# Kernel optimization log

Hardware: AMD Instinct MI355X
Metric: run time of the kernel (lower is better)

Reference implementation:

```python
import jax, jax.numpy as jnp
import numpy as np

D_MODEL = 256
N_HEADS = 8
N_LEVELS = 4
NUM_POINTS_LIST = [4, 4, 4, 4]
SUM_POINTS = sum(NUM_POINTS_LIST)
TOTAL_POINTS = N_HEADS * SUM_POINTS
HEAD_DIM = D_MODEL // N_HEADS
OFFSET_SCALE = 0.5
SPATIAL_SHAPES = np.array([[80, 80], [40, 40], [20, 20], [10, 10]], dtype=np.int64)


def setup_inputs() -> dict:
    key = jax.random.key(0)
    ks = jax.random.split(key, 7)
    B, NQ = 16, 300
    seq = int((SPATIAL_SHAPES[:, 0] * SPATIAL_SHAPES[:, 1]).sum())  # 8500
    s = 1.0 / np.sqrt(D_MODEL)
    return {
        'hidden_states': jax.random.normal(ks[0], (B, NQ, D_MODEL), jnp.float32),
        'encoder_hidden_states': jax.random.normal(ks[1], (B, seq, D_MODEL), jnp.float32),
        'reference_points': jax.random.uniform(ks[2], (B, NQ, 1, 4), jnp.float32, 0.05, 0.95),
        'spatial_shapes': SPATIAL_SHAPES,
        'w_off': jax.random.uniform(ks[3], (TOTAL_POINTS * 2, D_MODEL), jnp.float32, -s, s),
        'b_off': jax.random.uniform(ks[4], (TOTAL_POINTS * 2,), jnp.float32, -s, s),
        'w_attn': jax.random.uniform(ks[5], (TOTAL_POINTS, D_MODEL), jnp.float32, -s, s),
        'b_attn': jax.random.uniform(ks[6], (TOTAL_POINTS,), jnp.float32, -s, s),
    }


def _grid_sample_zeros(img_flat, H, W, gx, gy):
    # img_flat: [N, H*W, C]; gx, gy: [N, Q, P] unnormalized pixel coords.
    # Bilinear, padding_mode='zeros', align_corners=False semantics of torch.grid_sample.
    x0 = jnp.floor(gx)
    y0 = jnp.floor(gy)
    wx = (gx - x0)[..., None]
    wy = (gy - y0)[..., None]
    x0i = x0.astype(jnp.int32)
    y0i = y0.astype(jnp.int32)

    def gather(xi, yi):
        valid = (xi >= 0) & (xi < W) & (yi >= 0) & (yi < H)
        idx = jnp.clip(yi, 0, H - 1) * W + jnp.clip(xi, 0, W - 1)
        N = img_flat.shape[0]
        v = jnp.take_along_axis(img_flat, idx.reshape(N, -1)[..., None], axis=1)
        v = v.reshape(idx.shape + (img_flat.shape[-1],))
        return v * valid[..., None]

    v00 = gather(x0i, y0i)
    v01 = gather(x0i + 1, y0i)
    v10 = gather(x0i, y0i + 1)
    v11 = gather(x0i + 1, y0i + 1)
    top = v00 * (1 - wx) + v01 * wx
    bot = v10 * (1 - wx) + v11 * wx
    return top * (1 - wy) + bot * wy  # [N, Q, P, C]


def reference(hidden_states, encoder_hidden_states, reference_points, spatial_shapes, w_off, b_off, w_attn, b_attn):
    B, NQ, _ = hidden_states.shape
    seq = encoder_hidden_states.shape[1]
    shapes = np.asarray(spatial_shapes)

    value = encoder_hidden_states.reshape(B, seq, N_HEADS, HEAD_DIM)

    off = (hidden_states @ w_off.T + b_off).reshape(B, NQ, N_HEADS, SUM_POINTS, 2)
    attn = jax.nn.softmax((hidden_states @ w_attn.T + b_attn).reshape(B, NQ, N_HEADS, SUM_POINTS), axis=-1)

    # reference_points: [B, NQ, 1, 4] (cx, cy, w, h) in [0,1]
    nps = jnp.asarray(np.repeat([1.0 / n for n in NUM_POINTS_LIST], NUM_POINTS_LIST), hidden_states.dtype)[:, None]
    offset = off * nps * reference_points[:, :, None, :, 2:] * OFFSET_SCALE
    sampling_locations = reference_points[:, :, None, :, :2] + offset  # [B,NQ,H,P,2]

    grids = 2.0 * sampling_locations - 1.0
    value_bh = value.transpose(0, 2, 1, 3).reshape(B * N_HEADS, seq, HEAD_DIM)
    grids_bh = grids.transpose(0, 2, 1, 3, 4).reshape(B * N_HEADS, NQ, SUM_POINTS, 2)

    outs = []
    start_s, start_p = 0, 0
    for lvl in range(N_LEVELS):
        Hl, Wl = int(shapes[lvl, 0]), int(shapes[lvl, 1])
        Pl = NUM_POINTS_LIST[lvl]
        img = value_bh[:, start_s:start_s + Hl * Wl]  # [BH, Hl*Wl, hd]
        g = grids_bh[:, :, start_p:start_p + Pl]
        gx = (g[..., 0] + 1.0) * Wl / 2.0 - 0.5
        gy = (g[..., 1] + 1.0) * Hl / 2.0 - 0.5
        outs.append(_grid_sample_zeros(img, Hl, Wl, gx, gy))
        start_s += Hl * Wl
        start_p += Pl

    sampled = jnp.concatenate(outs, axis=2)  # [BH, NQ, SUM_POINTS, hd]
    attn_bh = attn.transpose(0, 2, 1, 3).reshape(B * N_HEADS, NQ, SUM_POINTS, 1)
    out = (sampled * attn_bh).sum(axis=2)  # [BH, NQ, hd]
    out = out.reshape(B, N_HEADS, NQ, HEAD_DIM).transpose(0, 2, 1, 3).reshape(B, NQ, D_MODEL)
    return (out, attn)
```

## Files before the change

### kernel.cpp

```cpp
#include <hip/hip_runtime.h>
#include <hip/hip_bf16.h>

#define BQ_TOTAL 4800
#define D_MODEL 256
#define N_HEADS 8
#define SUM_POINTS 16
#define HEAD_DIM 32
#define SEQ 8500
#define OUT_ELEMS (BQ_TOTAL * D_MODEL)
#define ATTN_ELEMS (BQ_TOTAL * N_HEADS * SUM_POINTS)

#define BM 64
#define BN 64
#define BK 32
#define PAD 4

__global__ __launch_bounds__(256) void gemm_logits(
    const float* __restrict__ hs,
    const float* __restrict__ w_off, const float* __restrict__ b_off,
    const float* __restrict__ w_attn, const float* __restrict__ b_attn,
    float* __restrict__ off_out, float* __restrict__ attn_out)
{
    __shared__ float As[BK][BM + PAD];
    __shared__ float Bs[BK][BN + PAD];

    const int tid = threadIdx.x;
    const int row0 = blockIdx.x * BM;
    const int col0 = blockIdx.y * BN;

    const float* Bsrc; const float* bias; int bcol;
    if (col0 < 256) { Bsrc = w_off;  bias = b_off;  bcol = col0; }
    else            { Bsrc = w_attn; bias = b_attn; bcol = col0 - 256; }

    const int tx = tid & 15;
    const int ty = tid >> 4;
    const int lrow = tid >> 3;
    const int k4 = (tid & 7) * 4;

    float acc[4][4] = {};

    for (int k0 = 0; k0 < 256; k0 += BK) {
        #pragma unroll
        for (int rr = 0; rr < 2; rr++) {
            const int r = lrow + rr * 32;
            const float4 a = *(const float4*)(hs + (size_t)(row0 + r) * 256 + k0 + k4);
            As[k4 + 0][r] = a.x; As[k4 + 1][r] = a.y;
            As[k4 + 2][r] = a.z; As[k4 + 3][r] = a.w;
            const float4 b = *(const float4*)(Bsrc + (size_t)(bcol + r) * 256 + k0 + k4);
            Bs[k4 + 0][r] = b.x; Bs[k4 + 1][r] = b.y;
            Bs[k4 + 2][r] = b.z; Bs[k4 + 3][r] = b.w;
        }
        __syncthreads();
        #pragma unroll
        for (int kk = 0; kk < BK; kk++) {
            const float4 av = *(const float4*)&As[kk][ty * 4];
            const float4 bv = *(const float4*)&Bs[kk][tx * 4];
            const float af[4] = {av.x, av.y, av.z, av.w};
            const float bf[4] = {bv.x, bv.y, bv.z, bv.w};
            #pragma unroll
            for (int i = 0; i < 4; i++)
                #pragma unroll
                for (int j = 0; j < 4; j++)
                    acc[i][j] += af[i] * bf[j];
        }
        __syncthreads();
    }

    #pragma unroll
    for (int i = 0; i < 4; i++) {
        const int r = row0 + ty * 4 + i;
        const int c_local = tx * 4;
        float4 v;
        v.x = acc[i][0] + bias[bcol + c_local + 0];
        v.y = acc[i][1] + bias[bcol + c_local + 1];
        v.z = acc[i][2] + bias[bcol + c_local + 2];
        v.w = acc[i][3] + bias[bcol + c_local + 3];
        if (col0 < 256)
            *(float4*)(off_out + (size_t)r * 256 + col0 + c_local) = v;
        else
            *(float4*)(attn_out + (size_t)r * 128 + (col0 - 256) + c_local) = v;
    }
}

__global__ __launch_bounds__(256) void deform_sample(
    const float* __restrict__ enc,
    const float* __restrict__ refp,
    const float* __restrict__ offlog,
    float* __restrict__ attn,
    float* __restrict__ out)
{
    __shared__ float probs[4][16];
    __shared__ float offs[4][32];

    const int tid = threadIdx.x;
    const int w = tid >> 6;
    const int lane = tid & 63;
    const int item = blockIdx.x * 4 + w;
    const int bq = item >> 3;
    const int h = item & 7;

    float* attn_ptr = attn + (size_t)bq * 128 + h * 16;
    if (lane < 16) {
        const float l = attn_ptr[lane];
        float m = l;
        #pragma unroll
        for (int s = 1; s < 16; s <<= 1) m = fmaxf(m, __shfl_xor(m, s, 16));
        const float e = __expf(l - m);
        float ssum = e;
        #pragma unroll
        for (int s = 1; s < 16; s <<= 1) ssum += __shfl_xor(ssum, s, 16);
        const float p = e / ssum;
        attn_ptr[lane] = p;
        probs[w][lane] = p;
    }
    if (lane < 32) {
        offs[w][lane] = offlog[(size_t)bq * 256 + h * 32 + lane];
    }
    const float* rp = refp + (size_t)bq * 4;
    const float cx = rp[0], cy = rp[1], rw = rp[2], rh = rp[3];
    __syncthreads();

    const int c = lane & 31;
    const int half = lane >> 5;
    const int b = bq / 300;
    const float* encb = enc + ((size_t)b * SEQ) * 256 + h * 32 + c;

    const int   Wl_[4]   = {80, 40, 20, 10};
    const int   base_[4] = {0, 6400, 8000, 8400};

    float acc = 0.f;
    #pragma unroll
    for (int p8 = 0; p8 < 8; p8++) {
        const int p = p8 * 2 + half;
        const int lvl = p >> 2;
        const int Wl = Wl_[lvl];
        const int base = base_[lvl];

        const float a  = probs[w][p];
        const float ox = offs[w][2 * p];
        const float oy = offs[w][2 * p + 1];
        const float lx = cx + ox * 0.125f * rw;
        const float ly = cy + oy * 0.125f * rh;
        const float gx = lx * (float)Wl - 0.5f;
        const float gy = ly * (float)Wl - 0.5f;
        const float x0f = floorf(gx), y0f = floorf(gy);
        const float fx = gx - x0f, fy = gy - y0f;
        const int x0 = (int)x0f, y0 = (int)y0f;

        const bool xv0 = (x0 >= 0) && (x0 < Wl);
        const bool xv1 = (x0 + 1 >= 0) && (x0 + 1 < Wl);
        const bool yv0 = (y0 >= 0) && (y0 < Wl);
        const bool yv1 = (y0 + 1 >= 0) && (y0 + 1 < Wl);

        float v00 = 0.f, v01 = 0.f, v10 = 0.f, v11 = 0.f;
        const float* rowp0 = encb + (size_t)(base + y0 * Wl) * 256;
        if (yv0) {
            if (xv0) v00 = rowp0[(size_t)x0 * 256];
            if (xv1) v01 = rowp0[(size_t)(x0 + 1) * 256];
        }
        if (yv1) {
            const float* rowp1 = rowp0 + (size_t)Wl * 256;
            if (xv0) v10 = rowp1[(size_t)x0 * 256];
            if (xv1) v11 = rowp1[(size_t)(x0 + 1) * 256];
        }
        const float top = v00 + (v01 - v00) * fx;
        const float bot = v10 + (v11 - v10) * fx;
        acc += a * (top + (bot - top) * fy);
    }
    acc += __shfl_xor(acc, 32);
    if (half == 0) {
        out[(size_t)bq * 256 + h * 32 + c] = acc;
    }
}

extern "C" void kernel_launch(void* const* d_in, const int* in_sizes, int n_in,
                              void* d_out, int out_size, void* d_ws, size_t ws_size,
                              hipStream_t stream) {
    const float* hs     = (const float*)d_in[0];
    const float* enc    = (const float*)d_in[1];
    const float* refp   = (const float*)d_in[2];
    const float* w_off  = (const float*)d_in[4];
    const float* b_off  = (const float*)d_in[5];
    const float* w_attn = (const float*)d_in[6];
    const float* b_attn = (const float*)d_in[7];

    float* out  = (float*)d_out;
    float* attn = out + OUT_ELEMS;
    float* offlog = (float*)d_ws;

    dim3 g1(BQ_TOTAL / BM, 384 / BN);
    gemm_logits<<<g1, 256, 0, stream>>>(hs, w_off, b_off, w_attn, b_attn, offlog, attn);

    deform_sample<<<(BQ_TOTAL * N_HEADS) / 4, 256, 0, stream>>>(enc, refp, offlog, attn, out);
}
```

Measured before the change: 236.3 us.

## Remap deform sampling lanes to point×channel-group with float4 gathers and shuffle reduction

The sampling kernel now gives each lane one sampling point and a group of 8 channels, loaded as two float4s per bilinear corner. The old mapping gave each lane one channel and looped over 8 points. Softmax and offsets are computed per lane through cross-lane shuffles, which removes the shared-memory staging and the __syncthreads. Out-of-bounds corners are clamped and zero-weighted, so loads are branchless. The cost is a 4-step xor-shuffle reduction across points for 8 values per lane, plus more redundant per-lane coordinate math.

```diff
diff --git a/kernel.cpp b/kernel.cpp
--- a/kernel.cpp
+++ b/kernel.cpp
@@ -8,7 +8,6 @@
 #define HEAD_DIM 32
 #define SEQ 8500
 #define OUT_ELEMS (BQ_TOTAL * D_MODEL)
-#define ATTN_ELEMS (BQ_TOTAL * N_HEADS * SUM_POINTS)
 
 #define BM 64
 #define BN 64
@@ -89,87 +88,91 @@
     float* __restrict__ attn,
     float* __restrict__ out)
 {
-    __shared__ float probs[4][16];
-    __shared__ float offs[4][32];
-
     const int tid = threadIdx.x;
     const int w = tid >> 6;
     const int lane = tid & 63;
     const int item = blockIdx.x * 4 + w;
     const int bq = item >> 3;
     const int h = item & 7;
+    const int p = lane >> 2;
+    const int sub = lane & 3;
 
     float* attn_ptr = attn + (size_t)bq * 128 + h * 16;
-    if (lane < 16) {
-        const float l = attn_ptr[lane];
-        float m = l;
-        #pragma unroll
-        for (int s = 1; s < 16; s <<= 1) m = fmaxf(m, __shfl_xor(m, s, 16));
-        const float e = __expf(l - m);
-        float ssum = e;
-        #pragma unroll
-        for (int s = 1; s < 16; s <<= 1) ssum += __shfl_xor(ssum, s, 16);
-        const float p = e / ssum;
-        attn_ptr[lane] = p;
-        probs[w][lane] = p;
-    }
-    if (lane < 32) {
-        offs[w][lane] = offlog[(size_t)bq * 256 + h * 32 + lane];
-    }
+    const float l = attn_ptr[p];
+    float m = l;
+    #pragma unroll
+    for (int s = 4; s < 64; s <<= 1) m = fmaxf(m, __shfl_xor(m, s));
+    const float e = __expf(l - m);
+    float ssum = e;
+    #pragma unroll
+    for (int s = 4; s < 64; s <<= 1) ssum += __shfl_xor(ssum, s);
+    const float prob = e / ssum;
+    if (sub == 0) attn_ptr[p] = prob;
+
+    const float2 off2 = *(const float2*)(offlog + (size_t)bq * 256 + h * 32 + 2 * p);
     const float* rp = refp + (size_t)bq * 4;
     const float cx = rp[0], cy = rp[1], rw = rp[2], rh = rp[3];
-    __syncthreads();
 
-    const int c = lane & 31;
-    const int half = lane >> 5;
+    const int lvl = p >> 2;
+    const int Wl = 80 >> lvl;
+    int base = 0;
+    if (lvl == 1) base = 6400;
+    else if (lvl == 2) base = 8000;
+    else if (lvl == 3) base = 8400;
+
+    const float Wf = (float)Wl;
+    const float gx = (cx + off2.x * 0.125f * rw) * Wf - 0.5f;
+    const float gy = (cy + off2.y * 0.125f * rh) * Wf - 0.5f;
+    const float x0f = floorf(gx), y0f = floorf(gy);
+    const float fx = gx - x0f, fy = gy - y0f;
+    const int x0 = (int)x0f, y0 = (int)y0f;
+
     const int b = bq / 300;
-    const float* encb = enc + ((size_t)b * SEQ) * 256 + h * 32 + c;
+    const float* pbase = enc + ((size_t)b * SEQ + base) * 256 + h * 32 + sub * 4;
 
-    const int   Wl_[4]   = {80, 40, 20, 10};
-    const int   base_[4] = {0, 6400, 8000, 8400};
+    float4 acc0 = {0.f, 0.f, 0.f, 0.f};
+    float4 acc1 = {0.f, 0.f, 0.f, 0.f};
+    #pragma unroll
+    for (int c = 0; c < 4; c++) {
+        const int xc = x0 + (c & 1);
+        const int yc = y0 + (c >> 1);
+        const float wx = (c & 1) ? fx : (1.0f - fx);
+        const float wy = (c >> 1) ? fy : (1.0f - fy);
+        const bool valid = (xc >= 0) && (xc < Wl) && (yc >= 0) && (yc < Wl);
+        const int xi = min(max(xc, 0), Wl - 1);
+        const int yi = min(max(yc, 0), Wl - 1);
+        const float wgt = valid ? wx * wy : 0.0f;
+        const float* vp = pbase + (size_t)(yi * Wl + xi) * 256;
+        const float4 va = *(const float4*)(vp);
+        const float4 vb = *(const float4*)(vp + 16);
+        acc0.x += wgt * va.x; acc0.y += wgt * va.y;
+        acc0.z += wgt * va.z; acc0.w += wgt * va.w;
+        acc1.x += wgt * vb.x; acc1.y += wgt * vb.y;
+        acc1.z += wgt * vb.z; acc1.w += wgt * vb.w;
+    }
 
-    float acc = 0.f;
+    float vals[8];
+    vals[0] = acc0.x * prob; vals[1] = acc0.y * prob;
+    vals[2] = acc0.z * prob; vals[3] = acc0.w * prob;
+    vals[4] = acc1.x * prob; vals[5] = acc1.y * prob;
+    vals[6] = acc1.z * prob; vals[7] = acc1.w * prob;
+
     #pragma unroll
-    for (int p8 = 0; p8 < 8; p8++) {
-        const int p = p8 * 2 + half;
-        const int lvl = p >> 2;
-        const int Wl = Wl_[lvl];
-        const int base = base_[lvl];
+    for (int s = 4; s < 64; s <<= 1) {
+        #pragma unroll
+        for (int j = 0; j < 8; j++) vals[j] += __shfl_xor(vals[j], s);
+    }
 
-        const float a  = probs[w][p];
-        const float ox = offs[w][2 * p];
-        const float oy = offs[w][2 * p + 1];
-        const float lx = cx + ox * 0.125f * rw;
-        const float ly = cy + oy * 0.125f * rh;
-        const float gx = lx * (float)Wl - 0.5f;
-        const float gy = ly * (float)Wl - 0.5f;
-        const float x0f = floorf(gx), y0f = floorf(gy);
-        const float fx = gx - x0f, fy = gy - y0f;
-        const int x0 = (int)x0f, y0 = (int)y0f;
-
-        const bool xv0 = (x0 >= 0) && (x0 < Wl);
-        const bool xv1 = (x0 + 1 >= 0) && (x0 + 1 < Wl);
-        const bool yv0 = (y0 >= 0) && (y0 < Wl);
-        const bool yv1 = (y0 + 1 >= 0) && (y0 + 1 < Wl);
-
-        float v00 = 0.f, v01 = 0.f, v10 = 0.f, v11 = 0.f;
-        const float* rowp0 = encb + (size_t)(base + y0 * Wl) * 256;
-        if (yv0) {
-            if (xv0) v00 = rowp0[(size_t)x0 * 256];
-            if (xv1) v01 = rowp0[(size_t)(x0 + 1) * 256];
-        }
-        if (yv1) {
-            const float* rowp1 = rowp0 + (size_t)Wl * 256;
-            if (xv0) v10 = rowp1[(size_t)x0 * 256];
-            if (xv1) v11 = rowp1[(size_t)(x0 + 1) * 256];
-        }
-        const float top = v00 + (v01 - v00) * fx;
-        const float bot = v10 + (v11 - v10) * fx;
-        acc += a * (top + (bot - top) * fy);
-    }
-    acc += __shfl_xor(acc, 32);
-    if (half == 0) {
-        out[(size_t)bq * 256 + h * 32 + c] = acc;
+    if (lane < 8) {
+        const int halfs = lane >> 2;
+        const int sb = lane & 3;
+        float4 v;
+        if (halfs == 0) { v.x = vals[0]; v.y = vals[1]; v.z = vals[2]; v.w = vals[3]; }
+        else            { v.x = vals[4]; v.y = vals[5]; v.z = vals[6]; v.w = vals[7]; }
+        out[(size_t)bq * 256 + h * 32 + halfs * 16 + sb * 4 + 0] = v.x;
+        out[(size_t)bq * 256 + h * 32 + halfs * 16 + sb * 4 + 1] = v.y;
+        out[(size_t)bq * 256 + h * 32 + halfs * 16 + sb * 4 + 2] = v.z;
+        out[(size_t)bq * 256 + h * 32 + halfs * 16 + sb * 4 + 3] = v.w;
     }
 }
 
```

Result: faster. 231.4 us (-2.0%).
